# Performance work log

Measured on AMD Instinct MI355X. Metric: run time of the kernel, lower is better.

## Reference

```python
import jax, jax.numpy as jnp
import numpy as np

KHS = 3        # kernel_half_size
SIGMA = 1.6    # sigma / dx
DX = 1.0
C = 20.0       # accumulate() hard-codes c = 20


def _gauss_kernel():
    size = 2 * KHS + 1
    g = np.arange(size, dtype=np.float32) - (size - 1) / 2.0
    g = np.exp(-(g / SIGMA) ** 2 / 2.0) / (SIGMA * np.sqrt(2.0 * np.pi))
    k = g[:, None, None] * g[None, :, None] * g[None, None, :]
    k = k / k.sum()
    return jnp.asarray(k[None, None], dtype=jnp.float32)  # [1,1,7,7,7]


def _smooth(x, kernel):
    # depthwise (single-channel) 3d gaussian conv, 'same' padding, zero bias
    return jax.lax.conv_general_dilated(
        x, kernel, window_strides=(1, 1, 1),
        padding=[(KHS, KHS)] * 3,
        dimension_numbers=("NCDHW", "OIDHW", "NCDHW"))


def _fdiff(f, axis):
    # forward difference, replicate last difference to keep size (torchJacobian3 style)
    d = jnp.diff(f, axis=axis)
    last = jax.lax.slice_in_dim(d, d.shape[axis] - 1, d.shape[axis], axis=axis)
    return jnp.concatenate([d, last], axis=axis)


def _curl(v):
    # v: [B,3,D,H,W]; per-channel fields are [B,D,H,W]; z->axis1, y->axis2, x->axis3
    u, vv, w = v[:, 0], v[:, 1], v[:, 2]
    cu = _fdiff(w, 2) - _fdiff(vv, 1)   # dw/dy - dv/dz
    cv = _fdiff(u, 1) - _fdiff(w, 3)    # du/dz - dw/dx
    cw = _fdiff(vv, 3) - _fdiff(u, 2)   # dv/dx - du/dy
    return jnp.stack([cu, cv, cw], axis=1)


def _integrate(t, v):
    # trapezoidal transmittance-weighted integral along depth (dim 2)
    front = (1.0 - t[:, :, 0]) * v[:, :, 0]
    trap = jnp.sum((t[:, :, :-1] - t[:, :, 1:]) * (v[:, :, :-1] + v[:, :, 1:]) * 0.5, axis=2)
    return front + trap


def setup_inputs() -> dict:
    key = jax.random.key(0)
    k1, k2 = jax.random.split(key)
    d = jax.random.uniform(k1, (4, 1, 128, 128, 128), dtype=jnp.float32)
    v = jax.random.normal(k2, (4, 3, 128, 128, 128), dtype=jnp.float32)
    return {"d": d, "v": v}


def reference(d, v):
    kern = _gauss_kernel()
    ds = _smooth(d, kern)
    vort = _curl(v) / DX
    vn = jnp.sqrt(jnp.sum(vort ** 2, axis=1, keepdims=True))  # [B,1,D,H,W]
    vn = _smooth(vn, kern)
    # single default view dir 'zp' -> identity rotation
    df = jnp.flip(ds, axis=2)
    vf = jnp.flip(vn, axis=2)
    x = jnp.cumsum(df * DX, axis=2)
    t = (x * C + 1.0) * jnp.exp(-C * x)
    iv = _integrate(t, vf)              # [B,1,H,W]
    return jnp.clip(iv, 0.0, 1.0)
```

## Files before the change

kernel.cpp:

```cpp
#include <hip/hip_runtime.h>
#include <math.h>

#define NB 4
#define DD 128
#define HH 128
#define WW 128
#define VOX (DD*HH*WW)
#define NVOX (NB*VOX)

struct GaussW { float w[7]; };

__device__ __forceinline__ float4 f4zero() { float4 z; z.x = z.y = z.z = z.w = 0.f; return z; }

__global__ void curl4_kernel(const float* __restrict__ v, float* __restrict__ vn) {
    int idx = blockIdx.x * blockDim.x + threadIdx.x;
    int xq = idx & 31;
    int y  = (idx >> 5) & 127;
    int z  = (idx >> 12) & 127;
    int n  = idx >> 19;
    int x0 = xq << 2;
    const float* u  = v + (size_t)n * 3 * VOX;
    const float* vv = u + VOX;
    const float* w  = vv + VOX;
    size_t s = ((size_t)z << 14) | ((size_t)y << 7) | (size_t)x0;

    int dy = (y < 127) ? 128 : -128;
    int dz = (z < 127) ? 16384 : -16384;
    float sy = (y < 127) ? 1.f : -1.f;
    float sz = (z < 127) ? 1.f : -1.f;
    int dxp = (xq < 31) ? 4 : 0;

    const float4 wc  = *(const float4*)(w  + s);
    const float4 wyn = *(const float4*)(w  + s + dy);
    const float4 vc  = *(const float4*)(vv + s);
    const float4 vzn = *(const float4*)(vv + s + dz);
    const float4 uc  = *(const float4*)(u  + s);
    const float4 uzn = *(const float4*)(u  + s + dz);
    const float4 uyn = *(const float4*)(u  + s + dy);
    const float  wxp = w [s + 3 + dxp];
    const float  vxp = vv[s + 3 + dxp];

    float wca[4] = {wc.x, wc.y, wc.z, wc.w};
    float vca[4] = {vc.x, vc.y, vc.z, vc.w};
    float wya[4] = {wyn.x, wyn.y, wyn.z, wyn.w};
    float vza[4] = {vzn.x, vzn.y, vzn.z, vzn.w};
    float uca[4] = {uc.x, uc.y, uc.z, uc.w};
    float uza[4] = {uzn.x, uzn.y, uzn.z, uzn.w};
    float uya[4] = {uyn.x, uyn.y, uyn.z, uyn.w};
    float wsh[4] = {wc.y, wc.z, wc.w, wxp};
    float vsh[4] = {vc.y, vc.z, vc.w, vxp};

    float4 o;
    float* oa = &o.x;
#pragma unroll
    for (int j = 0; j < 4; ++j) {
        int x = x0 + j;
        float fdxw = (x < 127) ? (wsh[j] - wca[j]) : (wca[3] - wca[2]);
        float fdxv = (x < 127) ? (vsh[j] - vca[j]) : (vca[3] - vca[2]);
        float fdyw = sy * (wya[j] - wca[j]);
        float fdyu = sy * (uya[j] - uca[j]);
        float fdzv = sz * (vza[j] - vca[j]);
        float fdzu = sz * (uza[j] - uca[j]);
        float cu = fdyw - fdzv;
        float cv = fdzu - fdxw;
        float cw = fdxv - fdyu;
        oa[j] = sqrtf(cu * cu + cv * cv + cw * cw);
    }
    *(float4*)(vn + ((size_t)n * VOX) + s) = o;
}

__global__ void yx_smooth4_dual_kernel(const float* __restrict__ inA, float* __restrict__ outA,
                                       const float* __restrict__ inB, float* __restrict__ outB,
                                       GaussW gw) {
    __shared__ float in_t[38][128];
    __shared__ float mid[32][136];

    int bb = blockIdx.x;
    const float* in  = (bb < 2048) ? inA  : inB;
    float*       out = (bb < 2048) ? outA : outB;
    int b  = bb & 2047;
    int yq = b & 3;
    int z  = (b >> 2) & 127;
    int n  = b >> 9;
    int y0 = yq * 32;
    size_t slice = (((size_t)n << 7) | (size_t)z) << 14;
    int tid = threadIdx.x;

    for (int j = tid; j < 38 * 32; j += 256) {
        int r  = j >> 5;
        int c4 = (j & 31) << 2;
        int gy = y0 - 3 + r;
        float4 val = (gy >= 0 && gy < 128)
                   ? *(const float4*)(in + slice + ((size_t)gy << 7) + c4)
                   : f4zero();
        *(float4*)&in_t[r][c4] = val;
    }
    __syncthreads();

    if (tid < 32) {
        *(float4*)&mid[tid][0]   = f4zero();
        *(float4*)&mid[tid][132] = f4zero();
    }
    for (int j = tid; j < 32 * 32; j += 256) {
        int yo = j >> 5;
        int c4 = (j & 31) << 2;
        float4 a = f4zero();
#pragma unroll
        for (int k = 0; k < 7; ++k) {
            float wk = gw.w[k];
            float4 t = *(const float4*)&in_t[yo + k][c4];
            a.x += wk * t.x; a.y += wk * t.y; a.z += wk * t.z; a.w += wk * t.w;
        }
        *(float4*)&mid[yo][c4 + 4] = a;
    }
    __syncthreads();

    for (int j = tid; j < 32 * 32; j += 256) {
        int yo  = j >> 5;
        int x0c = (j & 31) << 2;
        float4 m0 = *(const float4*)&mid[yo][x0c];
        float4 m1 = *(const float4*)&mid[yo][x0c + 4];
        float4 m2 = *(const float4*)&mid[yo][x0c + 8];
        float wdw[12] = {m0.x, m0.y, m0.z, m0.w,
                         m1.x, m1.y, m1.z, m1.w,
                         m2.x, m2.y, m2.z, m2.w};
        float o[4];
#pragma unroll
        for (int j2 = 0; j2 < 4; ++j2) {
            float acc = 0.f;
#pragma unroll
            for (int k = 0; k < 7; ++k) acc += gw.w[k] * wdw[j2 + 1 + k];
            o[j2] = acc;
        }
        *(float4*)(out + slice + ((size_t)(y0 + yo) << 7) + x0c) =
            make_float4(o[0], o[1], o[2], o[3]);
    }
}

#define RBATCH 16
__global__ __launch_bounds__(256, 2)
void render_zs_kernel(const float* __restrict__ P, const float* __restrict__ Q,
                      float* __restrict__ out, GaussW gw) {
    int idx = blockIdx.x * blockDim.x + threadIdx.x;
    if (idx >= NB * HH * WW) return;
    int x = idx & 127;
    int y = (idx >> 7) & 127;
    int n = idx >> 14;
    size_t volbase = (size_t)n * VOX + ((size_t)y << 7) + x;

    float pc[6], qc[6];
#pragma unroll
    for (int t = 0; t < 3; ++t) { pc[t] = 0.f; qc[t] = 0.f; }
#pragma unroll
    for (int t = 3; t < 6; ++t) {
        int j = t - 3;
        size_t off = volbase + ((size_t)(127 - j) << 14);
        pc[t] = P[off];
        qc[t] = Q[off];
    }

    float xacc = 0.f, acc = 0.f, tp = 0.f, vp = 0.f;
    for (int b = 0; b < 128 / RBATCH; ++b) {
        int j0 = b * RBATCH;
        float pw[RBATCH + 6], qw[RBATCH + 6];
#pragma unroll
        for (int t = 0; t < 6; ++t) { pw[t] = pc[t]; qw[t] = qc[t]; }
#pragma unroll
        for (int i = 0; i < RBATCH; ++i) {
            int j = j0 + 3 + i;
            if (j <= 127) {
                size_t off = volbase + ((size_t)(127 - j) << 14);
                pw[6 + i] = P[off];
                qw[6 + i] = Q[off];
            } else {
                pw[6 + i] = 0.f;
                qw[6 + i] = 0.f;
            }
        }
#pragma unroll
        for (int i = 0; i < RBATCH; ++i) {
            float dsf = 0.f, vnf = 0.f;
#pragma unroll
            for (int k = 0; k < 7; ++k) {
                float wk = gw.w[k];
                dsf += wk * pw[i + k];
                vnf += wk * qw[i + k];
            }
            xacc += dsf;
            float xc = 20.f * xacc;
            float tk = (xc + 1.f) * __expf(-xc);
            if (j0 + i == 0) acc = (1.f - tk) * vnf;
            else             acc += (tp - tk) * (vp + vnf) * 0.5f;
            tp = tk; vp = vnf;
        }
#pragma unroll
        for (int t = 0; t < 6; ++t) { pc[t] = pw[RBATCH + t]; qc[t] = qw[RBATCH + t]; }
    }
    out[idx] = fminf(fmaxf(acc, 0.f), 1.f);
}

extern "C" void kernel_launch(void* const* d_in, const int* in_sizes, int n_in,
                              void* d_out, int out_size, void* d_ws, size_t ws_size,
                              hipStream_t stream) {
    const float* d = (const float*)d_in[0];
    const float* v = (const float*)d_in[1];
    float* out = (float*)d_out;

    GaussW gw;
    {
        double g[7], s = 0.0;
        for (int i = 0; i < 7; ++i) {
            double t = (i - 3) / 1.6;
            g[i] = exp(-t * t / 2.0);
            s += g[i];
        }
        for (int i = 0; i < 7; ++i) gw.w[i] = (float)(g[i] / s);
    }

    float* ws0 = (float*)d_ws;
    float* ws1 = ws0 + NVOX;
    float* ws2 = ws1 + NVOX;

    const int TB = 256;

    curl4_kernel<<<(NVOX / 4) / TB, TB, 0, stream>>>(v, ws1);

    yx_smooth4_dual_kernel<<<2 * NB * DD * 4, TB, 0, stream>>>(d, ws0, ws1, ws2, gw);

    render_zs_kernel<<<(NB * HH * WW) / TB, TB, 0, stream>>>(ws0, ws2, out, gw);
}
```

Measured before the change: 212.2 us.

## Fuse curl magnitude computation into the y/x smoothing kernel

The separate curl kernel is removed. The smoothing kernel's curl blocks now compute vorticity magnitude straight into shared memory, recomputing it for the 3-row y halo. This drops a full-volume write and re-read of the vorticity norm and one kernel launch. In exchange, halo rows are recomputed (38/32 overhead on curl loads) and launch bounds rise to 4 blocks per SM, which may add register pressure.

```diff
diff --git a/kernel.cpp b/kernel.cpp
--- a/kernel.cpp
+++ b/kernel.cpp
@@ -12,18 +12,12 @@
 
 __device__ __forceinline__ float4 f4zero() { float4 z; z.x = z.y = z.z = z.w = 0.f; return z; }
 
-__global__ void curl4_kernel(const float* __restrict__ v, float* __restrict__ vn) {
-    int idx = blockIdx.x * blockDim.x + threadIdx.x;
-    int xq = idx & 31;
-    int y  = (idx >> 5) & 127;
-    int z  = (idx >> 12) & 127;
-    int n  = idx >> 19;
-    int x0 = xq << 2;
-    const float* u  = v + (size_t)n * 3 * VOX;
-    const float* vv = u + VOX;
-    const float* w  = vv + VOX;
+__device__ __forceinline__ float4 curl4_at(const float* __restrict__ u,
+                                           const float* __restrict__ vv,
+                                           const float* __restrict__ w,
+                                           int z, int y, int x0) {
+    int xq = x0 >> 2;
     size_t s = ((size_t)z << 14) | ((size_t)y << 7) | (size_t)x0;
-
     int dy = (y < 127) ? 128 : -128;
     int dz = (z < 127) ? 16384 : -16384;
     float sy = (y < 127) ? 1.f : -1.f;
@@ -66,18 +60,18 @@
         float cw = fdxv - fdyu;
         oa[j] = sqrtf(cu * cu + cv * cv + cw * cw);
     }
-    *(float4*)(vn + ((size_t)n * VOX) + s) = o;
-}
-
-__global__ void yx_smooth4_dual_kernel(const float* __restrict__ inA, float* __restrict__ outA,
-                                       const float* __restrict__ inB, float* __restrict__ outB,
-                                       GaussW gw) {
+    return o;
+}
+
+__global__ __launch_bounds__(256, 4)
+void yx_curl_dual_kernel(const float* __restrict__ dIn, float* __restrict__ P,
+                         const float* __restrict__ v,   float* __restrict__ Q,
+                         GaussW gw) {
     __shared__ float in_t[38][128];
     __shared__ float mid[32][136];
 
     int bb = blockIdx.x;
-    const float* in  = (bb < 2048) ? inA  : inB;
-    float*       out = (bb < 2048) ? outA : outB;
+    bool isCurl = (bb >= 2048);
     int b  = bb & 2047;
     int yq = b & 3;
     int z  = (b >> 2) & 127;
@@ -86,14 +80,29 @@
     size_t slice = (((size_t)n << 7) | (size_t)z) << 14;
     int tid = threadIdx.x;
 
-    for (int j = tid; j < 38 * 32; j += 256) {
-        int r  = j >> 5;
-        int c4 = (j & 31) << 2;
-        int gy = y0 - 3 + r;
-        float4 val = (gy >= 0 && gy < 128)
-                   ? *(const float4*)(in + slice + ((size_t)gy << 7) + c4)
-                   : f4zero();
-        *(float4*)&in_t[r][c4] = val;
+    if (!isCurl) {
+        for (int j = tid; j < 38 * 32; j += 256) {
+            int r  = j >> 5;
+            int c4 = (j & 31) << 2;
+            int gy = y0 - 3 + r;
+            float4 val = (gy >= 0 && gy < 128)
+                       ? *(const float4*)(dIn + slice + ((size_t)gy << 7) + c4)
+                       : f4zero();
+            *(float4*)&in_t[r][c4] = val;
+        }
+    } else {
+        const float* u  = v + (size_t)n * 3 * VOX;
+        const float* vv = u + VOX;
+        const float* w  = vv + VOX;
+        for (int j = tid; j < 38 * 32; j += 256) {
+            int r  = j >> 5;
+            int c4 = (j & 31) << 2;
+            int gy = y0 - 3 + r;
+            float4 val = (gy >= 0 && gy < 128)
+                       ? curl4_at(u, vv, w, z, gy, c4)
+                       : f4zero();
+            *(float4*)&in_t[r][c4] = val;
+        }
     }
     __syncthreads();
 
@@ -115,6 +124,7 @@
     }
     __syncthreads();
 
+    float* out = isCurl ? Q : P;
     for (int j = tid; j < 32 * 32; j += 256) {
         int yo  = j >> 5;
         int x0c = (j & 31) << 2;
@@ -219,13 +229,10 @@
 
     float* ws0 = (float*)d_ws;
     float* ws1 = ws0 + NVOX;
-    float* ws2 = ws1 + NVOX;
 
     const int TB = 256;
 
-    curl4_kernel<<<(NVOX / 4) / TB, TB, 0, stream>>>(v, ws1);
-
-    yx_smooth4_dual_kernel<<<2 * NB * DD * 4, TB, 0, stream>>>(d, ws0, ws1, ws2, gw);
-
-    render_zs_kernel<<<(NB * HH * WW) / TB, TB, 0, stream>>>(ws0, ws2, out, gw);
-}
+    yx_curl_dual_kernel<<<2 * NB * DD * 4, TB, 0, stream>>>(d, ws0, v, ws1, gw);
+
+    render_zs_kernel<<<(NB * HH * WW) / TB, TB, 0, stream>>>(ws0, ws1, out, gw);
+}
```

After: 202.8 us. -4.4%, faster.
